# Performance work log

Measured on AMD Instinct MI355X. Metric: run time of the kernel, lower is better.

## Reference

```python
import jax, jax.numpy as jnp
import numpy as np

NX, NY = 512, 512
DX, DY = 1e-4, 1e-4
VS = 1550.0
DT = 2.5e-8


def setup_inputs() -> dict:
    key = jax.random.key(0)
    k1, k2 = jax.random.split(key)
    sensor_data = jax.random.normal(k1, (4, 2, 128, 2048), dtype=jnp.float32)
    sensor_xy = jax.random.randint(k2, (128, 2), 0, 512, dtype=jnp.int32)
    return {"sensor_data": sensor_data, "sensor_xy": sensor_xy}


def _delay_indices(sensor_xy):
    # pixel grids, 1-indexed as in the torch code (arange(1,513))
    ix = jnp.arange(1, NX + 1, dtype=jnp.float32)[None, :, None]  # (1,Nx,1)
    iy = jnp.arange(1, NY + 1, dtype=jnp.float32)[None, None, :]  # (1,1,Ny)
    x = sensor_xy[:, 0].astype(jnp.float32)[:, None, None]        # (S,1,1)
    y = sensor_xy[:, 1].astype(jnp.float32)[:, None, None]
    dis = jnp.sqrt(((x - ix + 1.0) * DX) ** 2 + ((y - iy + 1.0) * DY) ** 2)  # (S,Nx,Ny)
    # .to(torch.long) truncates; values are non-negative so int cast matches
    return (dis / VS / DT).astype(jnp.int32).reshape(sensor_xy.shape[0], -1)  # (S, Nx*Ny)


def reference(sensor_data, sensor_xy):
    B = sensor_data.shape[0]
    S = sensor_xy.shape[0]
    t = _delay_indices(sensor_xy)                           # (S, P) int32
    data = jnp.transpose(sensor_data, (2, 0, 1, 3))         # (S, B, 2, T)

    def step(img, xs):
        t_s, d_s = xs                                       # (P,), (B,2,T)
        return img + d_s[:, :, t_s], None                   # gather + accumulate

    img0 = jnp.zeros((B, 2, NX * NY), dtype=sensor_data.dtype)
    img, _ = jax.lax.scan(step, img0, (t, data))
    return img.reshape(B, 2, NX, NY)
```

## Files before the change

kernel.cpp:

```cpp
#include <hip/hip_runtime.h>
#include <math.h>


#define NXY 512
#define S_CNT 128
#define T_CNT 2048
#define CH 8
#define CH_STRIDE (S_CNT * T_CNT)
#define NPIX (NXY * NXY)
#define TAB_BYTES (NPIX * 2)

#pragma float_control(push)
#pragma float_control(precise, on)
__device__ __forceinline__ unsigned short delay_entry(int adx, int ady) {
    const double DX32 = (double)1e-4f;
    const double R1 = (double)(float)(1.0 / 1550.0);
    const double R2 = (double)(float)(1.0 / (double)2.5e-8f);
    float dxf = (float)((double)adx * DX32);
    float dyf = (float)((double)ady * DX32);
    float a2 = (float)((double)dxf * (double)dxf);
    float b2 = (float)((double)dyf * (double)dyf);
    float sum = (float)((double)a2 + (double)b2);
    float dis = (float)sqrt((double)sum);
    float q1 = (float)((double)dis * R1);
    float q2 = (float)((double)q1 * R2);
    return (unsigned short)(int)q2;
}

__device__ __forceinline__ unsigned int bf16_rne(float f) {
    unsigned int x = __float_as_uint(f);
    return (x + 0x7fffu + ((x >> 16) & 1u)) >> 16;
}

__global__ __launch_bounds__(256) void prep(const float* __restrict__ data,
                                            unsigned short* __restrict__ tab,
                                            uint4* __restrict__ d2b) {
    int idx = blockIdx.x * 256 + threadIdx.x;
    tab[idx] = delay_entry(idx >> 9, idx & 511);

    unsigned int w[4];
#pragma unroll
    for (int j = 0; j < 4; ++j) {
        unsigned int lo = bf16_rne(data[(2 * j) * CH_STRIDE + idx]);
        unsigned int hi = bf16_rne(data[(2 * j + 1) * CH_STRIDE + idx]);
        w[j] = lo | (hi << 16);
    }
    d2b[idx] = make_uint4(w[0], w[1], w[2], w[3]);
}
#pragma float_control(pop)

__device__ __forceinline__ float bflo(unsigned int u) { return __uint_as_float(u << 16); }
__device__ __forceinline__ float bfhi(unsigned int u) { return __uint_as_float(u & 0xffff0000u); }

__global__ __launch_bounds__(256) void das_gather8b(const uint4* __restrict__ d2b,
                                                    const unsigned short* __restrict__ tab,
                                                    const int* __restrict__ sxy,
                                                    float* __restrict__ out) {
    __shared__ int sx[S_CNT];
    __shared__ int sy[S_CNT];
    int tid = threadIdx.x;
    if (tid < S_CNT) {
        sx[tid] = sxy[2 * tid];
        sy[tid] = sxy[2 * tid + 1];
    }
    __syncthreads();

    int iy = ((blockIdx.x & 31) << 4) | (((tid >> 6) & 1) << 3) | (tid & 7);
    int ix = ((blockIdx.x >> 5) << 4) | ((tid >> 7) << 3) | ((tid >> 3) & 7);

    float acc[CH];
#pragma unroll
    for (int k = 0; k < CH; ++k) acc[k] = 0.0f;

#pragma unroll 4
    for (int s = 0; s < S_CNT; ++s) {
        int dxi = sx[s] - ix;
        int dyi = sy[s] - iy;
        int adx = dxi < 0 ? -dxi : dxi;
        int ady = dyi < 0 ? -dyi : dyi;
        int t = (int)tab[(adx << 9) | ady];
        uint4 w = d2b[(s << 11) + t];
        acc[0] += bflo(w.x);
        acc[1] += bfhi(w.x);
        acc[2] += bflo(w.y);
        acc[3] += bfhi(w.y);
        acc[4] += bflo(w.z);
        acc[5] += bfhi(w.z);
        acc[6] += bflo(w.w);
        acc[7] += bfhi(w.w);
    }

    int pix = (ix << 9) | iy;
#pragma unroll
    for (int k = 0; k < CH; ++k) out[k * NPIX + pix] = acc[k];
}

#pragma float_control(push)
#pragma float_control(precise, on)
__global__ __launch_bounds__(256) void build_table(unsigned short* __restrict__ tab) {
    int idx = blockIdx.x * 256 + threadIdx.x;
    tab[idx] = delay_entry(idx >> 9, idx & 511);
}
#pragma float_control(pop)

__global__ __launch_bounds__(256) void das_main(const float* __restrict__ data,
                                                const unsigned short* __restrict__ tab,
                                                const int* __restrict__ sxy,
                                                float* __restrict__ out) {
    __shared__ int sx[S_CNT];
    __shared__ int sy[S_CNT];
    int tid = threadIdx.x;
    if (tid < S_CNT) {
        sx[tid] = sxy[2 * tid];
        sy[tid] = sxy[2 * tid + 1];
    }
    __syncthreads();
    int iy = ((blockIdx.x & 31) << 4) | (tid & 15);
    int ix = ((blockIdx.x >> 5) << 4) | (tid >> 4);
    float acc[CH];
#pragma unroll
    for (int k = 0; k < CH; ++k) acc[k] = 0.0f;
#pragma unroll 4
    for (int s = 0; s < S_CNT; ++s) {
        int dxi = sx[s] - ix;
        int dyi = sy[s] - iy;
        int adx = dxi < 0 ? -dxi : dxi;
        int ady = dyi < 0 ? -dyi : dyi;
        int t = (int)tab[(adx << 9) | ady];
        const float* p = data + (s << 11) + t;
#pragma unroll
        for (int k = 0; k < CH; ++k) acc[k] += p[(size_t)k * CH_STRIDE];
    }
    int pix = (ix << 9) | iy;
#pragma unroll
    for (int k = 0; k < CH; ++k) out[k * NPIX + pix] = acc[k];
}

extern "C" void kernel_launch(void* const* d_in, const int* in_sizes, int n_in,
                              void* d_out, int out_size, void* d_ws, size_t ws_size,
                              hipStream_t stream) {
    const float* data = (const float*)d_in[0];
    const int* sxy = (const int*)d_in[1];
    float* out = (float*)d_out;
    unsigned short* tab = (unsigned short*)d_ws;

    size_t need = (size_t)TAB_BYTES + (size_t)CH_STRIDE * 16;
    if (ws_size >= need) {
        uint4* d2b = (uint4*)((char*)d_ws + TAB_BYTES);
        prep<<<NPIX / 256, 256, 0, stream>>>(data, tab, d2b);
        das_gather8b<<<1024, 256, 0, stream>>>(d2b, tab, sxy, out);
    } else {
        build_table<<<NPIX / 256, 256, 0, stream>>>(tab);
        das_main<<<1024, 256, 0, stream>>>(data, tab, sxy, out);
    }
}
```

Measured before the change: 96.76 us.

## Compute two adjacent pixels per thread sharing one delay-table load; vectorize prep

The gather kernel now gives each thread two neighbouring y-pixels. Their two delay entries are adjacent in the table, so one 8-byte table read plus some select logic serves both. Each thread issues two bf16-packed sample gathers per sensor and writes its results as float2 stores. The grid is halved, which adds independent loads per thread but doubles accumulator registers. The prep kernel now handles four elements per thread using float4 loads and ushort4 table stores.

```diff
diff --git a/kernel.cpp b/kernel.cpp
--- a/kernel.cpp
+++ b/kernel.cpp
@@ -35,27 +35,38 @@
 __global__ __launch_bounds__(256) void prep(const float* __restrict__ data,
                                             unsigned short* __restrict__ tab,
                                             uint4* __restrict__ d2b) {
-    int idx = blockIdx.x * 256 + threadIdx.x;
-    tab[idx] = delay_entry(idx >> 9, idx & 511);
+    int i0 = (blockIdx.x * 256 + threadIdx.x) * 4;
+    int adx = i0 >> 9;
+    int ady0 = i0 & 511;
+    ushort4 te;
+    te.x = delay_entry(adx, ady0);
+    te.y = delay_entry(adx, ady0 + 1);
+    te.z = delay_entry(adx, ady0 + 2);
+    te.w = delay_entry(adx, ady0 + 3);
+    *(ushort4*)(tab + i0) = te;
 
-    unsigned int w[4];
+    float4 v[CH];
+#pragma unroll
+    for (int k = 0; k < CH; ++k) v[k] = *(const float4*)(data + k * CH_STRIDE + i0);
 #pragma unroll
     for (int j = 0; j < 4; ++j) {
-        unsigned int lo = bf16_rne(data[(2 * j) * CH_STRIDE + idx]);
-        unsigned int hi = bf16_rne(data[(2 * j + 1) * CH_STRIDE + idx]);
-        w[j] = lo | (hi << 16);
+        const float* c = (const float*)v;
+        unsigned int w0 = bf16_rne(c[0 * 4 + j]) | (bf16_rne(c[1 * 4 + j]) << 16);
+        unsigned int w1 = bf16_rne(c[2 * 4 + j]) | (bf16_rne(c[3 * 4 + j]) << 16);
+        unsigned int w2 = bf16_rne(c[4 * 4 + j]) | (bf16_rne(c[5 * 4 + j]) << 16);
+        unsigned int w3 = bf16_rne(c[6 * 4 + j]) | (bf16_rne(c[7 * 4 + j]) << 16);
+        d2b[i0 + j] = make_uint4(w0, w1, w2, w3);
     }
-    d2b[idx] = make_uint4(w[0], w[1], w[2], w[3]);
 }
 #pragma float_control(pop)
 
 __device__ __forceinline__ float bflo(unsigned int u) { return __uint_as_float(u << 16); }
 __device__ __forceinline__ float bfhi(unsigned int u) { return __uint_as_float(u & 0xffff0000u); }
 
-__global__ __launch_bounds__(256) void das_gather8b(const uint4* __restrict__ d2b,
-                                                    const unsigned short* __restrict__ tab,
-                                                    const int* __restrict__ sxy,
-                                                    float* __restrict__ out) {
+__global__ __launch_bounds__(256) void das_gather2(const uint4* __restrict__ d2b,
+                                                   const unsigned short* __restrict__ tab,
+                                                   const int* __restrict__ sxy,
+                                                   float* __restrict__ out) {
     __shared__ int sx[S_CNT];
     __shared__ int sy[S_CNT];
     int tid = threadIdx.x;
@@ -65,34 +76,58 @@
     }
     __syncthreads();
 
-    int iy = ((blockIdx.x & 31) << 4) | (((tid >> 6) & 1) << 3) | (tid & 7);
-    int ix = ((blockIdx.x >> 5) << 4) | ((tid >> 7) << 3) | ((tid >> 3) & 7);
+    int bx = blockIdx.x & 31;
+    int by = blockIdx.x >> 5;
+    int ix = (bx << 4) | ((tid >> 7) << 3) | ((tid >> 3) & 7);
+    int iy0 = (by << 5) | (((tid >> 6) & 1) << 4) | ((tid & 7) << 1);
 
-    float acc[CH];
+    float acc0[CH], acc1[CH];
 #pragma unroll
-    for (int k = 0; k < CH; ++k) acc[k] = 0.0f;
+    for (int k = 0; k < CH; ++k) { acc0[k] = 0.0f; acc1[k] = 0.0f; }
+
+    const char* tabb = (const char*)tab;
 
 #pragma unroll 4
     for (int s = 0; s < S_CNT; ++s) {
         int dxi = sx[s] - ix;
-        int dyi = sy[s] - iy;
         int adx = dxi < 0 ? -dxi : dxi;
-        int ady = dyi < 0 ? -dyi : dyi;
-        int t = (int)tab[(adx << 9) | ady];
-        uint4 w = d2b[(s << 11) + t];
-        acc[0] += bflo(w.x);
-        acc[1] += bfhi(w.x);
-        acc[2] += bflo(w.y);
-        acc[3] += bfhi(w.y);
-        acc[4] += bflo(w.z);
-        acc[5] += bfhi(w.z);
-        acc[6] += bflo(w.w);
-        acc[7] += bfhi(w.w);
+        int dy0 = sy[s] - iy0;
+        int ady0 = dy0 < 0 ? -dy0 : dy0;
+        int dy1 = dy0 - 1;
+        int ady1 = dy1 < 0 ? -dy1 : dy1;
+        int m = ady0 < ady1 ? ady0 : ady1;
+        int boff = (((adx << 9) + m) << 1) & ~3;
+        uint2 d = *(const uint2*)(tabb + boff);
+        unsigned sel = (unsigned)(m & 1);
+        unsigned em = sel ? (d.x >> 16) : (d.x & 0xffffu);
+        unsigned em1 = sel ? (d.y & 0xffffu) : (d.x >> 16);
+        unsigned t0 = (ady0 == m) ? em : em1;
+        unsigned t1 = (ady0 == m) ? em1 : em;
+        uint4 w0 = d2b[(s << 11) + t0];
+        uint4 w1 = d2b[(s << 11) + t1];
+        acc0[0] += bflo(w0.x);
+        acc0[1] += bfhi(w0.x);
+        acc0[2] += bflo(w0.y);
+        acc0[3] += bfhi(w0.y);
+        acc0[4] += bflo(w0.z);
+        acc0[5] += bfhi(w0.z);
+        acc0[6] += bflo(w0.w);
+        acc0[7] += bfhi(w0.w);
+        acc1[0] += bflo(w1.x);
+        acc1[1] += bfhi(w1.x);
+        acc1[2] += bflo(w1.y);
+        acc1[3] += bfhi(w1.y);
+        acc1[4] += bflo(w1.z);
+        acc1[5] += bfhi(w1.z);
+        acc1[6] += bflo(w1.w);
+        acc1[7] += bfhi(w1.w);
     }
 
-    int pix = (ix << 9) | iy;
+    int pix = (ix << 9) | iy0;
 #pragma unroll
-    for (int k = 0; k < CH; ++k) out[k * NPIX + pix] = acc[k];
+    for (int k = 0; k < CH; ++k) {
+        *(float2*)(out + k * NPIX + pix) = make_float2(acc0[k], acc1[k]);
+    }
 }
 
 #pragma float_control(push)
@@ -147,8 +182,8 @@
     size_t need = (size_t)TAB_BYTES + (size_t)CH_STRIDE * 16;
     if (ws_size >= need) {
         uint4* d2b = (uint4*)((char*)d_ws + TAB_BYTES);
-        prep<<<NPIX / 256, 256, 0, stream>>>(data, tab, d2b);
-        das_gather8b<<<1024, 256, 0, stream>>>(d2b, tab, sxy, out);
+        prep<<<NPIX / 1024, 256, 0, stream>>>(data, tab, d2b);
+        das_gather2<<<512, 256, 0, stream>>>(d2b, tab, sxy, out);
     } else {
         build_table<<<NPIX / 256, 256, 0, stream>>>(tab);
         das_main<<<1024, 256, 0, stream>>>(data, tab, sxy, out);
```

After: 105.2 us. 8.8% more time.

## Stage per-sensor sample windows in LDS and vectorize prep kernel

Applied to the files above, without the earlier changes.

The main kernel now computes, for each group of 8 sensors, the minimum delay over the block's 16x16 pixel tile. It loads a 64-sample window of packed bf16 data starting at that delay into shared memory with coalesced reads, and each pixel then gathers from LDS instead of scattered global loads. The window width relies on the delay spread across a 16x16 tile staying under 64 samples, and it adds two block barriers per sensor group. The prep kernel now handles 4 elements per thread with float4/ushort4 vector accesses and launches a quarter as many blocks.

```diff
diff --git a/kernel.cpp b/kernel.cpp
--- a/kernel.cpp
+++ b/kernel.cpp
@@ -35,29 +35,42 @@
 __global__ __launch_bounds__(256) void prep(const float* __restrict__ data,
                                             unsigned short* __restrict__ tab,
                                             uint4* __restrict__ d2b) {
-    int idx = blockIdx.x * 256 + threadIdx.x;
-    tab[idx] = delay_entry(idx >> 9, idx & 511);
+    int i0 = (blockIdx.x * 256 + threadIdx.x) * 4;
+    int adx = i0 >> 9;
+    int ady0 = i0 & 511;
+    ushort4 te;
+    te.x = delay_entry(adx, ady0);
+    te.y = delay_entry(adx, ady0 + 1);
+    te.z = delay_entry(adx, ady0 + 2);
+    te.w = delay_entry(adx, ady0 + 3);
+    *(ushort4*)(tab + i0) = te;
 
-    unsigned int w[4];
+    float4 v[CH];
+#pragma unroll
+    for (int k = 0; k < CH; ++k) v[k] = *(const float4*)(data + k * CH_STRIDE + i0);
 #pragma unroll
     for (int j = 0; j < 4; ++j) {
-        unsigned int lo = bf16_rne(data[(2 * j) * CH_STRIDE + idx]);
-        unsigned int hi = bf16_rne(data[(2 * j + 1) * CH_STRIDE + idx]);
-        w[j] = lo | (hi << 16);
+        const float* c = (const float*)v;
+        unsigned int w0 = bf16_rne(c[0 * 4 + j]) | (bf16_rne(c[1 * 4 + j]) << 16);
+        unsigned int w1 = bf16_rne(c[2 * 4 + j]) | (bf16_rne(c[3 * 4 + j]) << 16);
+        unsigned int w2 = bf16_rne(c[4 * 4 + j]) | (bf16_rne(c[5 * 4 + j]) << 16);
+        unsigned int w3 = bf16_rne(c[6 * 4 + j]) | (bf16_rne(c[7 * 4 + j]) << 16);
+        d2b[i0 + j] = make_uint4(w0, w1, w2, w3);
     }
-    d2b[idx] = make_uint4(w[0], w[1], w[2], w[3]);
 }
 #pragma float_control(pop)
 
 __device__ __forceinline__ float bflo(unsigned int u) { return __uint_as_float(u << 16); }
 __device__ __forceinline__ float bfhi(unsigned int u) { return __uint_as_float(u & 0xffff0000u); }
 
-__global__ __launch_bounds__(256) void das_gather8b(const uint4* __restrict__ d2b,
-                                                    const unsigned short* __restrict__ tab,
-                                                    const int* __restrict__ sxy,
-                                                    float* __restrict__ out) {
+__global__ __launch_bounds__(256) void das_stage(const uint4* __restrict__ d2b,
+                                                 const unsigned short* __restrict__ tab,
+                                                 const int* __restrict__ sxy,
+                                                 float* __restrict__ out) {
     __shared__ int sx[S_CNT];
     __shared__ int sy[S_CNT];
+    __shared__ int tmins[8];
+    __shared__ uint4 win[8][64];
     int tid = threadIdx.x;
     if (tid < S_CNT) {
         sx[tid] = sxy[2 * tid];
@@ -65,29 +78,50 @@
     }
     __syncthreads();
 
-    int iy = ((blockIdx.x & 31) << 4) | (((tid >> 6) & 1) << 3) | (tid & 7);
-    int ix = ((blockIdx.x >> 5) << 4) | ((tid >> 7) << 3) | ((tid >> 3) & 7);
+    int bx = blockIdx.x & 31;
+    int by = blockIdx.x >> 5;
+    int ix0 = bx << 4, iy0 = by << 4;
+    int iy = iy0 | (((tid >> 6) & 1) << 3) | (tid & 7);
+    int ix = ix0 | ((tid >> 7) << 3) | ((tid >> 3) & 7);
+    int wv = tid >> 6;
+    int lane = tid & 63;
 
     float acc[CH];
 #pragma unroll
     for (int k = 0; k < CH; ++k) acc[k] = 0.0f;
 
-#pragma unroll 4
-    for (int s = 0; s < S_CNT; ++s) {
-        int dxi = sx[s] - ix;
-        int dyi = sy[s] - iy;
-        int adx = dxi < 0 ? -dxi : dxi;
-        int ady = dyi < 0 ? -dyi : dyi;
-        int t = (int)tab[(adx << 9) | ady];
-        uint4 w = d2b[(s << 11) + t];
-        acc[0] += bflo(w.x);
-        acc[1] += bfhi(w.x);
-        acc[2] += bflo(w.y);
-        acc[3] += bfhi(w.y);
-        acc[4] += bflo(w.z);
-        acc[5] += bfhi(w.z);
-        acc[6] += bflo(w.w);
-        acc[7] += bfhi(w.w);
+    for (int b = 0; b < S_CNT / 8; ++b) {
+        __syncthreads();
+#pragma unroll
+        for (int jj = 0; jj < 2; ++jj) {
+            int j = (wv << 1) | jj;
+            int s = (b << 3) | j;
+            int sxv = sx[s], syv = sy[s];
+            int axmin = sxv < ix0 ? ix0 - sxv : (sxv > ix0 + 15 ? sxv - (ix0 + 15) : 0);
+            int aymin = syv < iy0 ? iy0 - syv : (syv > iy0 + 15 ? syv - (iy0 + 15) : 0);
+            int tmin = (int)delay_entry(axmin, aymin);
+            win[j][lane] = d2b[(s << 11) + tmin + lane];
+            if (lane == 0) tmins[j] = tmin;
+        }
+        __syncthreads();
+#pragma unroll
+        for (int j = 0; j < 8; ++j) {
+            int s = (b << 3) | j;
+            int dxi = sx[s] - ix;
+            int dyi = sy[s] - iy;
+            int adx = dxi < 0 ? -dxi : dxi;
+            int ady = dyi < 0 ? -dyi : dyi;
+            int t = (int)tab[(adx << 9) | ady];
+            uint4 w = win[j][t - tmins[j]];
+            acc[0] += bflo(w.x);
+            acc[1] += bfhi(w.x);
+            acc[2] += bflo(w.y);
+            acc[3] += bfhi(w.y);
+            acc[4] += bflo(w.z);
+            acc[5] += bfhi(w.z);
+            acc[6] += bflo(w.w);
+            acc[7] += bfhi(w.w);
+        }
     }
 
     int pix = (ix << 9) | iy;
@@ -147,8 +181,8 @@
     size_t need = (size_t)TAB_BYTES + (size_t)CH_STRIDE * 16;
     if (ws_size >= need) {
         uint4* d2b = (uint4*)((char*)d_ws + TAB_BYTES);
-        prep<<<NPIX / 256, 256, 0, stream>>>(data, tab, d2b);
-        das_gather8b<<<1024, 256, 0, stream>>>(d2b, tab, sxy, out);
+        prep<<<NPIX / 1024, 256, 0, stream>>>(data, tab, d2b);
+        das_stage<<<1024, 256, 0, stream>>>(d2b, tab, sxy, out);
     } else {
         build_table<<<NPIX / 256, 256, 0, stream>>>(tab);
         das_main<<<1024, 256, 0, stream>>>(data, tab, sxy, out);
```

Result: slower. 105.3 us (+8.8%).
